# Kernel tuning notes

Hardware: AMD Instinct MI355X
Metric: run time of the kernel (lower is better)

The kernel has to match this reference:

```python
import jax, jax.numpy as jnp
import numpy as np

N = 4096   # nodes
E = 65536  # edges
D_IN = 64
H = 128
T = 8
B = 8


def setup_inputs() -> dict:
    key = jax.random.key(0)
    ks = jax.random.split(key, 6)
    x = jax.random.normal(ks[0], (B, T, N, D_IN), jnp.float32)
    edge_index = jax.random.randint(ks[1], (2, E), 0, N, dtype=jnp.int32)
    W0 = jax.random.normal(ks[2], (D_IN + H, 4 * H), jnp.float32) * 0.05
    b0 = jax.random.normal(ks[3], (4 * H,), jnp.float32) * 0.05
    W1 = jax.random.normal(ks[4], (H + H, 4 * H), jnp.float32) * 0.05
    b1 = jax.random.normal(ks[5], (4 * H,), jnp.float32) * 0.05
    return {"x": x, "W0": W0, "b0": b0, "W1": W1, "b1": b1, "edge_index": edge_index}


def _gcn_norm(edge_index, n):
    # PyG GCNConv(improved=True): A_hat = A + 2I, deg over incoming edges (col)
    src, dst = edge_index[0], edge_index[1]
    deg = jax.ops.segment_sum(jnp.ones(edge_index.shape[1], jnp.float32), dst, num_segments=n) + 2.0
    dinv = jax.lax.rsqrt(deg)  # deg >= 2 always, safe
    return src, dst, dinv


def _gcn_gates(comb, W, b, src, dst, dinv, n):
    # comb: (b, n, i+h) -> gates: (b, n, 4h)
    xw = jnp.einsum('bnf,fg->bng', comb, W)
    norm_e = dinv[src] * dinv[dst]                      # (E,)
    msgs = xw[:, src, :] * norm_e[None, :, None]        # (b, E, 4h)
    agg = jax.vmap(lambda m: jax.ops.segment_sum(m, dst, num_segments=n))(msgs)
    # self-loop with weight 2: norm = 2 * dinv[i]^2
    agg = agg + (2.0 * dinv * dinv)[None, :, None] * xw + b
    return agg


def reference(x, W0, b0, W1, b1, edge_index):
    src, dst, dinv = _gcn_norm(edge_index, N)

    def run_layer(seq, W, b):
        h_dim = W.shape[1] // 4

        def step(carry, xt):
            h, c = carry
            comb = jnp.concatenate([xt, h], axis=-1)
            gates = _gcn_gates(comb, W, b, src, dst, dinv, N)
            ci, cf, co, cg = jnp.split(gates, 4, axis=-1)
            i = jax.nn.sigmoid(ci)
            f = jax.nn.sigmoid(cf)
            o = jax.nn.sigmoid(co)
            g = jnp.tanh(cg)
            c_next = f * c + i * g
            h_next = o * jnp.tanh(c_next)
            return (h_next, c_next), h_next

        h0 = jnp.zeros((seq.shape[1], N, h_dim), seq.dtype)
        _, hs = jax.lax.scan(step, (h0, h0), seq)
        return hs  # (t, b, n, h)

    seq = jnp.swapaxes(x, 0, 1)  # batch_first -> (t, b, n, d)
    hs0 = run_layer(seq, W0, b0)
    hs1 = run_layer(hs0, W1, b1)
    return jnp.swapaxes(hs1, 0, 1)  # (b, t, n, h) last-layer output sequence
```

## Files before the change

kernel.cpp:

```cpp
#include <hip/hip_runtime.h>
#include <hip/hip_fp16.h>
#include <math.h>

constexpr int N_NODES = 4096;
constexpr int N_EDGES = 65536;
constexpr int D_INF   = 64;
constexpr int H       = 128;
constexpr int T       = 8;
constexpr int B       = 8;
constexpr int M       = B * N_NODES;

typedef __attribute__((ext_vector_type(8))) short bf16x8;
typedef __attribute__((ext_vector_type(4))) float f32x4;
typedef __attribute__((ext_vector_type(8))) _Float16 f16x8;
typedef __attribute__((ext_vector_type(4))) _Float16 f16x4;

__device__ inline unsigned short f2bf(float x) {
  unsigned int u = __float_as_uint(x);
  unsigned int r = (u + 0x7fffu + ((u >> 16) & 1u)) >> 16;
  return (unsigned short)r;
}
__device__ inline float bf2f(unsigned short b) {
  return __uint_as_float((unsigned int)b << 16);
}
__device__ __forceinline__ int swz(int s) { return s ^ (((s >> 7) & 7) << 3); }


__global__ void k_count(const int* __restrict__ dst, int* __restrict__ cnt) {
  int e = blockIdx.x * blockDim.x + threadIdx.x;
  if (e < N_EDGES) atomicAdd(&cnt[dst[e]], 1);
}

__global__ void k_dinv(const int* __restrict__ cnt, float* __restrict__ dinv) {
  int n = blockIdx.x * blockDim.x + threadIdx.x;
  if (n < N_NODES) dinv[n] = 1.0f / sqrtf((float)cnt[n] + 2.0f);
}

__global__ void k_scan(const int* __restrict__ cnt, int* __restrict__ rowptr) {
  __shared__ int sums[1024];
  int t = threadIdx.x;
  int v0 = cnt[4*t+0], v1 = cnt[4*t+1], v2 = cnt[4*t+2], v3 = cnt[4*t+3];
  int s0 = v0, s1 = s0 + v1, s2 = s1 + v2, s3 = s2 + v3;
  sums[t] = s3;
  __syncthreads();
  for (int off = 1; off < 1024; off <<= 1) {
    int x = (t >= off) ? sums[t - off] : 0;
    __syncthreads();
    sums[t] += x;
    __syncthreads();
  }
  int base = (t > 0) ? sums[t - 1] : 0;
  if (t == 0) rowptr[0] = 0;
  rowptr[4*t+1] = base + s0;
  rowptr[4*t+2] = base + s1;
  rowptr[4*t+3] = base + s2;
  rowptr[4*t+4] = base + s3;
}

__global__ void k_fill(const int* __restrict__ src, const int* __restrict__ dst,
                       const float* __restrict__ dinv, const int* __restrict__ rowptr,
                       int* __restrict__ fill, int2* __restrict__ eg) {
  int e = blockIdx.x * blockDim.x + threadIdx.x;
  if (e >= N_EDGES) return;
  int s = src[e], d = dst[e];
  int p = rowptr[d] + atomicAdd(&fill[d], 1);
  eg[p] = make_int2(s, __float_as_int(dinv[s] * dinv[d]));
}

__global__ void k_hist(const int* __restrict__ cnt, int* __restrict__ hist) {
  int n = blockIdx.x * blockDim.x + threadIdx.x;
  if (n < N_NODES) atomicAdd(&hist[min(cnt[n], 127)], 1);
}

__global__ void k_hscan(const int* __restrict__ hist, int* __restrict__ hbase) {
  __shared__ int sh[128];
  int t = threadIdx.x;
  sh[t] = hist[t];
  __syncthreads();
  for (int off = 1; off < 128; off <<= 1) {
    int x = (t >= off) ? sh[t - off] : 0;
    __syncthreads();
    sh[t] += x;
    __syncthreads();
  }
  hbase[t] = sh[t] - hist[t];
}

__global__ void k_place(const int* __restrict__ cnt, const int* __restrict__ hbase,
                        int* __restrict__ filld, int* __restrict__ sorted) {
  int n = blockIdx.x * blockDim.x + threadIdx.x;
  if (n >= N_NODES) return;
  int d = min(cnt[n], 127);
  sorted[hbase[d] + atomicAdd(&filld[d], 1)] = n;
}

__global__ void k_pack(const float* __restrict__ W, unsigned short* __restrict__ Bp,
                       int K) {
  int tid = blockIdx.x * 256 + threadIdx.x;
  if (tid >= K * 64) return;
  int lane = tid & 63;
  int ntg  = (tid >> 6) & 31;
  int kb   = tid >> 11;
  int gate = ntg & 3, fg = ntg >> 2;
  int corig = gate * 128 + fg * 16 + (lane & 15);
  int k0 = kb * 32 + (lane >> 4) * 8;
  long obase = ((long)(kb * 32 + ntg) * 64 + lane) * 8;
  long plane = (long)K * 512;
  #pragma unroll
  for (int j = 0; j < 8; ++j) {
    float v = W[(long)(k0 + j) * 512 + corig];
    unsigned short h = f2bf(v);
    Bp[obase + j]         = h;
    Bp[plane + obase + j] = f2bf(v - bf2f(h));
  }
}

__global__ __launch_bounds__(256) void k_ax(
    const int* __restrict__ rowptr, const int2* __restrict__ eg,
    const float* __restrict__ dinv, const float* __restrict__ x,
    _Float16* __restrict__ AX) {
  int tid = threadIdx.x;
  int grp = blockIdx.x * 16 + (tid >> 4);
  int l   = tid & 15;
  int c4  = l * 4;
  int n   = grp & (N_NODES - 1);
  int bt  = grp >> 12;
  int b   = bt & 7, tt = bt >> 3;
  const float* Xb = x + (long)(b * T + tt) * N_NODES * D_INF;
  float acc[4] = {0.f, 0.f, 0.f, 0.f};
  int rs = rowptr[n], re = rowptr[n + 1];
  int e = rs;
  for (; e + 3 < re; e += 4) {
    int2 q0 = eg[e], q1 = eg[e + 1], q2 = eg[e + 2], q3 = eg[e + 3];
    float w0 = __int_as_float(q0.y), w1 = __int_as_float(q1.y);
    float w2 = __int_as_float(q2.y), w3 = __int_as_float(q3.y);
    f32x4 a0 = *(const f32x4*)(Xb + (long)q0.x * D_INF + c4);
    f32x4 a1 = *(const f32x4*)(Xb + (long)q1.x * D_INF + c4);
    f32x4 a2 = *(const f32x4*)(Xb + (long)q2.x * D_INF + c4);
    f32x4 a3 = *(const f32x4*)(Xb + (long)q3.x * D_INF + c4);
    #pragma unroll
    for (int q = 0; q < 4; ++q)
      acc[q] += w0 * a0[q] + w1 * a1[q] + w2 * a2[q] + w3 * a3[q];
  }
  for (; e < re; ++e) {
    int2 q0 = eg[e];
    float w0 = __int_as_float(q0.y);
    f32x4 a0 = *(const f32x4*)(Xb + (long)q0.x * D_INF + c4);
    #pragma unroll
    for (int q = 0; q < 4; ++q) acc[q] += w0 * a0[q];
  }
  float dn = dinv[n];
  float sw = 2.0f * dn * dn;
  f32x4 a = *(const f32x4*)(Xb + (long)n * D_INF + c4);
  #pragma unroll
  for (int q = 0; q < 4; ++q) acc[q] += sw * a[q];
  f16x4 o;
  #pragma unroll
  for (int q = 0; q < 4; ++q) o[q] = (_Float16)acc[q];
  *(f16x4*)(AX + ((long)(tt * 8 + b) * N_NODES + n) * D_INF + c4) = o;
}

__global__ __launch_bounds__(512, 4) void k_l0(
    const int* __restrict__ sorted,
    const _Float16* __restrict__ AXt,
    const unsigned short* __restrict__ AH0,
    const unsigned short* __restrict__ Bp, const float* __restrict__ bias,
    _Float16* __restrict__ hout, float* __restrict__ cbuf) {
  __shared__ __align__(16) unsigned short Atx[8 * 2 * 64 * 8];
  __shared__ int nodeLDS[64];
  int tid  = threadIdx.x;
  int lane = tid & 63;
  int w    = tid >> 6;
  int j    = blockIdx.x;
  int b    = j & 7;
  int jj   = j >> 3;
  int g    = lane >> 4, l = lane & 15;
  int c4   = l * 4;
  int kbA32  = c4 >> 5;
  int subA32 = (l & 7) >> 1;
  int j0A32  = (l & 1) * 4;

  #pragma unroll
  for (int nd = 0; nd < 2; ++nd) {
    int r = (w << 3) + (g << 1) + nd;
    int pairIdx = jj * 32 + (r >> 1);
    int n = (r & 1) ? sorted[N_NODES - 1 - pairIdx] : sorted[pairIdx];
    if (l == 0) nodeLDS[r] = n;
    f16x4 xv = *(const f16x4*)(AXt + ((long)b * N_NODES + n) * D_INF + c4);
    unsigned long long hv = 0ull, lv = 0ull;
    #pragma unroll
    for (int q = 0; q < 4; ++q) {
      float a = (float)xv[q];
      unsigned short hs = f2bf(a);
      unsigned short ls = f2bf(a - bf2f(hs));
      hv |= (unsigned long long)hs << (16 * q);
      lv |= (unsigned long long)ls << (16 * q);
    }
    int mt = r >> 4;
    int lA = (r & 15) + 16 * subA32;
    *(unsigned long long*)(Atx + swz(((mt * 2 + kbA32) * 64 + lA) * 8 + j0A32)) = hv;
    *(unsigned long long*)(Atx + swz((((4 + mt) * 2 + kbA32) * 64 + lA) * 8 + j0A32)) = lv;
  }
  __syncthreads();

  int l15 = lane & 15, lq = lane >> 4;
  const unsigned short* bb  = Bp + (long)(w * 4) * 512 + lane * 8;
  const unsigned short* blp = bb + (long)192 * 512;

  f32x4 acc[4][4];
  #pragma unroll
  for (int mt = 0; mt < 4; ++mt)
    #pragma unroll
    for (int gt = 0; gt < 4; ++gt)
      acc[mt][gt] = (f32x4){0.f, 0.f, 0.f, 0.f};

  __builtin_amdgcn_s_setprio(1);
  #pragma unroll
  for (int kb = 0; kb < 6; ++kb) {
    bf16x8 AH_[4], AL_[4];
    if (kb < 2) {
      #pragma unroll
      for (int mt = 0; mt < 4; ++mt) {
        AH_[mt] = *(const bf16x8*)(Atx + swz(((mt * 2 + kb) * 64 + lane) * 8));
        AL_[mt] = *(const bf16x8*)(Atx + swz((((4 + mt) * 2 + kb) * 64 + lane) * 8));
      }
    } else {
      #pragma unroll
      for (int mt = 0; mt < 4; ++mt) {
        AH_[mt] = *(const bf16x8*)(AH0 + ((((long)j * 8 + mt) * 4 + (kb - 2)) * 64 + lane) * 8);
        AL_[mt] = *(const bf16x8*)(AH0 + ((((long)j * 8 + 4 + mt) * 4 + (kb - 2)) * 64 + lane) * 8);
      }
    }
    bf16x8 BH[4], BL[4];
    #pragma unroll
    for (int gt = 0; gt < 4; ++gt) {
      BH[gt] = *(const bf16x8*)(bb  + ((long)kb * 32 + gt) * 512);
      BL[gt] = *(const bf16x8*)(blp + ((long)kb * 32 + gt) * 512);
    }
    #pragma unroll
    for (int gt = 0; gt < 4; ++gt) {
      #pragma unroll
      for (int mt = 0; mt < 4; ++mt) {
        acc[mt][gt] = __builtin_amdgcn_mfma_f32_16x16x32_bf16(AH_[mt], BH[gt], acc[mt][gt], 0, 0, 0);
        acc[mt][gt] = __builtin_amdgcn_mfma_f32_16x16x32_bf16(AL_[mt], BH[gt], acc[mt][gt], 0, 0, 0);
        acc[mt][gt] = __builtin_amdgcn_mfma_f32_16x16x32_bf16(AH_[mt], BL[gt], acc[mt][gt], 0, 0, 0);
      }
    }
  }
  __builtin_amdgcn_s_setprio(0);

  int f = w * 16 + l15;
  float bi = bias[f], bff = bias[128 + f], bo = bias[256 + f], bg = bias[384 + f];
  #pragma unroll
  for (int mt = 0; mt < 4; ++mt) {
    #pragma unroll
    for (int r = 0; r < 4; ++r) {
      int rt = mt * 16 + lq * 4 + r;
      int n2 = nodeLDS[rt];
      float vi = 1.0f / (1.0f + __expf(-(acc[mt][0][r] + bi)));
      float vf = 1.0f / (1.0f + __expf(-(acc[mt][1][r] + bff)));
      float vo = 1.0f / (1.0f + __expf(-(acc[mt][2][r] + bo)));
      float vg = tanhf(acc[mt][3][r] + bg);
      long idx = ((long)b * N_NODES + n2) * H + f;
      float cn = vf * cbuf[idx] + vi * vg;
      float hn = vo * tanhf(cn);
      cbuf[idx] = cn;
      hout[idx] = (_Float16)hn;
    }
  }
}

__global__ __launch_bounds__(512, 4) void k_l1(
    const int* __restrict__ rowptr, const int2* __restrict__ eg,
    const float* __restrict__ dinv, const int* __restrict__ sorted,
    const _Float16* __restrict__ H0,
    const _Float16* __restrict__ H1r,
    const unsigned short* __restrict__ Bp, const float* __restrict__ bias,
    unsigned short* __restrict__ AH0,
    _Float16* __restrict__ h1out, float* __restrict__ cbuf,
    float* __restrict__ out2, int t) {
  constexpr int KB = 8;
  __shared__ __align__(16) unsigned short At[8 * KB * 64 * 8];
  __shared__ int nodeLDS[64];
  int tid  = threadIdx.x;
  int lane = tid & 63;
  int w    = tid >> 6;
  int j    = blockIdx.x;
  int b    = j & 7;
  int jj   = j >> 3;
  int g    = lane >> 4, l = lane & 15;
  int c8   = l * 8;
  const _Float16* A_p = H0  + (long)b * N_NODES * H;
  const _Float16* B_p = H1r + (long)b * N_NODES * H;
  int lane2f = 16 * (l & 3);
  int kbA16  = c8 >> 5;
  int kbB    = 4 + kbA16;

  #pragma unroll
  for (int nd = 0; nd < 2; ++nd) {
    int r  = (w << 3) + (g << 1) + nd;
    int pairIdx = jj * 32 + (r >> 1);
    int n  = (r & 1) ? sorted[N_NODES - 1 - pairIdx] : sorted[pairIdx];
    if (l == 0) nodeLDS[r] = n;
    int rs = rowptr[n], re = rowptr[n + 1];
    float accA[8] = {0.f,0.f,0.f,0.f,0.f,0.f,0.f,0.f};
    float accB[8] = {0.f,0.f,0.f,0.f,0.f,0.f,0.f,0.f};
    int e = rs;
    for (; e + 3 < re; e += 4) {
      int2 q0 = eg[e], q1 = eg[e + 1], q2 = eg[e + 2], q3 = eg[e + 3];
      float w0 = __int_as_float(q0.y), w1 = __int_as_float(q1.y);
      float w2 = __int_as_float(q2.y), w3 = __int_as_float(q3.y);
      f16x8 a0 = *(const f16x8*)(A_p + (long)q0.x * H + c8);
      f16x8 a1 = *(const f16x8*)(A_p + (long)q1.x * H + c8);
      f16x8 a2 = *(const f16x8*)(A_p + (long)q2.x * H + c8);
      f16x8 a3 = *(const f16x8*)(A_p + (long)q3.x * H + c8);
      #pragma unroll
      for (int q = 0; q < 8; ++q)
        accA[q] += w0 * (float)a0[q] + w1 * (float)a1[q]
                 + w2 * (float)a2[q] + w3 * (float)a3[q];
      f16x8 b0 = *(const f16x8*)(B_p + (long)q0.x * H + c8);
      f16x8 b1 = *(const f16x8*)(B_p + (long)q1.x * H + c8);
      f16x8 b2 = *(const f16x8*)(B_p + (long)q2.x * H + c8);
      f16x8 b3 = *(const f16x8*)(B_p + (long)q3.x * H + c8);
      #pragma unroll
      for (int q = 0; q < 8; ++q)
        accB[q] += w0 * (float)b0[q] + w1 * (float)b1[q]
                 + w2 * (float)b2[q] + w3 * (float)b3[q];
    }
    for (; e < re; ++e) {
      int2 q0 = eg[e];
      float w0 = __int_as_float(q0.y);
      f16x8 a0 = *(const f16x8*)(A_p + (long)q0.x * H + c8);
      #pragma unroll
      for (int q = 0; q < 8; ++q) accA[q] += w0 * (float)a0[q];
      f16x8 b0 = *(const f16x8*)(B_p + (long)q0.x * H + c8);
      #pragma unroll
      for (int q = 0; q < 8; ++q) accB[q] += w0 * (float)b0[q];
    }
    float dn = dinv[n];
    float sw = 2.0f * dn * dn;
    {
      f16x8 a = *(const f16x8*)(A_p + (long)n * H + c8);
      f16x8 v = *(const f16x8*)(B_p + (long)n * H + c8);
      #pragma unroll
      for (int q = 0; q < 8; ++q) {
        accA[q] += sw * (float)a[q];
        accB[q] += sw * (float)v[q];
      }
    }

    int mt    = r >> 4;
    int lane2 = (r & 15) + lane2f;
    {
      bf16x8 hv, lv;
      #pragma unroll
      for (int q = 0; q < 8; ++q) {
        unsigned short hs = f2bf(accB[q]);
        hv[q] = (short)hs;
        lv[q] = (short)f2bf(accB[q] - bf2f(hs));
      }
      *(bf16x8*)(At + swz((((mt)     * KB + kbB) * 64 + lane2) * 8)) = hv;
      *(bf16x8*)(At + swz((((4 + mt) * KB + kbB) * 64 + lane2) * 8)) = lv;
    }
    {
      bf16x8 hv, lv;
      #pragma unroll
      for (int q = 0; q < 8; ++q) {
        unsigned short hs = f2bf(accA[q]);
        hv[q] = (short)hs;
        lv[q] = (short)f2bf(accA[q] - bf2f(hs));
      }
      *(bf16x8*)(At + swz((((mt)     * KB + kbA16) * 64 + lane2) * 8)) = hv;
      *(bf16x8*)(At + swz((((4 + mt) * KB + kbA16) * 64 + lane2) * 8)) = lv;
      *(bf16x8*)(AH0 + ((((long)j * 8 + mt)     * 4 + kbA16) * 64 + lane2) * 8) = hv;
      *(bf16x8*)(AH0 + ((((long)j * 8 + 4 + mt) * 4 + kbA16) * 64 + lane2) * 8) = lv;
    }
  }
  __syncthreads();

  int l15 = lane & 15, lq = lane >> 4;
  const unsigned short* bb  = Bp + (long)(w * 4) * 512 + lane * 8;
  const unsigned short* blp = bb + (long)256 * 512;

  f32x4 acc[4][4];
  #pragma unroll
  for (int mt = 0; mt < 4; ++mt)
    #pragma unroll
    for (int gt = 0; gt < 4; ++gt)
      acc[mt][gt] = (f32x4){0.f, 0.f, 0.f, 0.f};

  __builtin_amdgcn_s_setprio(1);
  #pragma unroll 2
  for (int kb = 0; kb < KB; ++kb) {
    bf16x8 AH_[4], AL_[4];
    #pragma unroll
    for (int mt = 0; mt < 4; ++mt) {
      AH_[mt] = *(const bf16x8*)(At + swz((((mt)     * KB + kb) * 64 + lane) * 8));
      AL_[mt] = *(const bf16x8*)(At + swz((((4 + mt) * KB + kb) * 64 + lane) * 8));
    }
    bf16x8 BH[4], BL[4];
    #pragma unroll
    for (int gt = 0; gt < 4; ++gt) {
      BH[gt] = *(const bf16x8*)(bb  + ((long)kb * 32 + gt) * 512);
      BL[gt] = *(const bf16x8*)(blp + ((long)kb * 32 + gt) * 512);
    }
    #pragma unroll
    for (int gt = 0; gt < 4; ++gt) {
      #pragma unroll
      for (int mt = 0; mt < 4; ++mt) {
        acc[mt][gt] = __builtin_amdgcn_mfma_f32_16x16x32_bf16(AH_[mt], BH[gt], acc[mt][gt], 0, 0, 0);
        acc[mt][gt] = __builtin_amdgcn_mfma_f32_16x16x32_bf16(AL_[mt], BH[gt], acc[mt][gt], 0, 0, 0);
        acc[mt][gt] = __builtin_amdgcn_mfma_f32_16x16x32_bf16(AH_[mt], BL[gt], acc[mt][gt], 0, 0, 0);
      }
    }
  }
  __builtin_amdgcn_s_setprio(0);

  int f = w * 16 + l15;
  float bi = bias[f], bff = bias[128 + f], bo = bias[256 + f], bg = bias[384 + f];
  #pragma unroll
  for (int mt = 0; mt < 4; ++mt) {
    #pragma unroll
    for (int r = 0; r < 4; ++r) {
      int rt = mt * 16 + lq * 4 + r;
      int n2 = nodeLDS[rt];
      float vi = 1.0f / (1.0f + __expf(-(acc[mt][0][r] + bi)));
      float vf = 1.0f / (1.0f + __expf(-(acc[mt][1][r] + bff)));
      float vo = 1.0f / (1.0f + __expf(-(acc[mt][2][r] + bo)));
      float vg = tanhf(acc[mt][3][r] + bg);
      long idx = ((long)b * N_NODES + n2) * H + f;
      float cn = vf * cbuf[idx] + vi * vg;
      float hn = vo * tanhf(cn);
      cbuf[idx] = cn;
      h1out[idx] = (_Float16)hn;
      __builtin_nontemporal_store(hn,
          &out2[(((long)b * T + t) * N_NODES + n2) * H + f]);
    }
  }
}


extern "C" void kernel_launch(void* const* d_in, const int* in_sizes, int n_in,
                              void* d_out, int out_size, void* d_ws, size_t ws_size,
                              hipStream_t stream) {
  const float* x  = (const float*)d_in[0];
  const float* W0 = (const float*)d_in[1];
  const float* b0 = (const float*)d_in[2];
  const float* W1 = (const float*)d_in[3];
  const float* b1 = (const float*)d_in[4];
  const int*   ei = (const int*)d_in[5];
  const int* srcp = ei;
  const int* dstp = ei + N_EDGES;
  float* out = (float*)d_out;

  char* p = (char*)d_ws;
  auto alloc = [&](size_t bytes) {
    char* r = p;
    p += (bytes + 255) & ~(size_t)255;
    return r;
  };
  int*   cnt    = (int*)  alloc(N_NODES * 4);
  int*   fill   = (int*)  alloc(N_NODES * 4);
  float* dinv   = (float*)alloc(N_NODES * 4);
  int*   rowptr = (int*)  alloc((N_NODES + 1) * 4);
  int2*  eg     = (int2*) alloc((size_t)N_EDGES * 8);
  int*   hist   = (int*)  alloc(128 * 4);
  int*   hbase  = (int*)  alloc(128 * 4);
  int*   filld  = (int*)  alloc(128 * 4);
  int*   sorted = (int*)  alloc(N_NODES * 4);
  float* cc     = (float*)alloc((size_t)2 * M * H * 4);
  _Float16* hh  = (_Float16*)alloc((size_t)3 * M * H * 2);
  _Float16* AX  = (_Float16*)alloc((size_t)T * M * D_INF * 2);
  unsigned short* AH0 = (unsigned short*)alloc((size_t)512 * 8 * 4 * 64 * 8 * 2);
  unsigned short* Bp0 = (unsigned short*)alloc((size_t)192 * 512 * 2 * 2);
  unsigned short* Bp1 = (unsigned short*)alloc((size_t)256 * 512 * 2 * 2);
  float*    c0  = cc;
  float*    c1  = cc + (size_t)M * H;
  _Float16* h0  = hh;
  _Float16* h1a = hh + (size_t)M * H;
  _Float16* h1b = hh + (size_t)2 * M * H;

  hipMemsetAsync(cnt,   0, N_NODES * 4, stream);
  hipMemsetAsync(fill,  0, N_NODES * 4, stream);
  hipMemsetAsync(hist,  0, 128 * 4, stream);
  hipMemsetAsync(filld, 0, 128 * 4, stream);
  hipMemsetAsync(cc,    0, (size_t)2 * M * H * 4, stream);
  hipMemsetAsync(hh,    0, (size_t)3 * M * H * 2, stream);
  hipMemsetAsync(AH0,   0, (size_t)512 * 8 * 4 * 64 * 8 * 2, stream);

  k_count<<<N_EDGES / 256, 256, 0, stream>>>(dstp, cnt);
  k_dinv <<<N_NODES / 256, 256, 0, stream>>>(cnt, dinv);
  k_scan <<<1, 1024, 0, stream>>>(cnt, rowptr);
  k_fill <<<N_EDGES / 256, 256, 0, stream>>>(srcp, dstp, dinv, rowptr, fill, eg);
  k_hist <<<N_NODES / 256, 256, 0, stream>>>(cnt, hist);
  k_hscan<<<1, 128, 0, stream>>>(hist, hbase);
  k_place<<<N_NODES / 256, 256, 0, stream>>>(cnt, hbase, filld, sorted);
  k_pack <<<(192 * 64 + 255) / 256, 256, 0, stream>>>(W0, Bp0, 192);
  k_pack <<<(256 * 64 + 255) / 256, 256, 0, stream>>>(W1, Bp1, 256);
  k_ax   <<<(8 * T * N_NODES) / 16, 256, 0, stream>>>(rowptr, eg, dinv, x, AX);

  for (int t = 0; t < T; ++t) {
    const _Float16* h1r = (t & 1) ? h1b : h1a;
    _Float16*       h1w = (t & 1) ? h1a : h1b;
    k_l0<<<512, 512, 0, stream>>>(sorted,
        AX + (size_t)t * M * D_INF, AH0, Bp0, b0, h0, c0);
    k_l1<<<512, 512, 0, stream>>>(rowptr, eg, dinv, sorted,
        h0, h1r, Bp1, b1, AH0, h1w, c1, out, t);
  }
}
```

Baseline: 829.5 us.

## Precompute A·X in MFMA-fragment bf16 hi/lo layout, batch all timesteps per edge

The A·X aggregation kernel now handles all 8 timesteps per node and batch, so each edge's index and weight are read once and reused across timesteps. It writes the result directly as split bf16 hi/lo fragments in the swizzle-free MFMA operand layout, indexed by each node's rank in the degree-sorted order, using a new rank kernel. The layer-0 step kernel therefore drops its LDS staging and per-step fp16-to-bf16 split conversion and loads A fragments straight from global memory. In exchange the AX buffer doubles in size, and k_ax keeps 32 accumulators per thread, which raises register pressure.

```diff
diff --git a/kernel.cpp b/kernel.cpp
--- a/kernel.cpp
+++ b/kernel.cpp
@@ -9,11 +9,11 @@
 constexpr int T       = 8;
 constexpr int B       = 8;
 constexpr int M       = B * N_NODES;
+constexpr long AXF_T  = 512L * 8 * 2 * 64 * 8;
 
 typedef __attribute__((ext_vector_type(8))) short bf16x8;
 typedef __attribute__((ext_vector_type(4))) float f32x4;
 typedef __attribute__((ext_vector_type(8))) _Float16 f16x8;
-typedef __attribute__((ext_vector_type(4))) _Float16 f16x4;
 
 __device__ inline unsigned short f2bf(float x) {
   unsigned int u = __float_as_uint(x);
@@ -94,6 +94,11 @@
   sorted[hbase[d] + atomicAdd(&filld[d], 1)] = n;
 }
 
+__global__ void k_rank(const int* __restrict__ sorted, int* __restrict__ rank) {
+  int p = blockIdx.x * 256 + threadIdx.x;
+  if (p < N_NODES) rank[sorted[p]] = p;
+}
+
 __global__ void k_pack(const float* __restrict__ W, unsigned short* __restrict__ Bp,
                        int K) {
   int tid = blockIdx.x * 256 + threadIdx.x;
@@ -115,58 +120,94 @@
   }
 }
 
-__global__ __launch_bounds__(256) void k_ax(
+__global__ void k_ax(
     const int* __restrict__ rowptr, const int2* __restrict__ eg,
-    const float* __restrict__ dinv, const float* __restrict__ x,
-    _Float16* __restrict__ AX) {
+    const float* __restrict__ dinv, const int* __restrict__ rank,
+    const float* __restrict__ x, unsigned short* __restrict__ AXf) {
   int tid = threadIdx.x;
-  int grp = blockIdx.x * 16 + (tid >> 4);
   int l   = tid & 15;
+  int b   = blockIdx.x & 7;
+  int n   = (blockIdx.x >> 3) * 16 + (tid >> 4);
   int c4  = l * 4;
-  int n   = grp & (N_NODES - 1);
-  int bt  = grp >> 12;
-  int b   = bt & 7, tt = bt >> 3;
-  const float* Xb = x + (long)(b * T + tt) * N_NODES * D_INF;
-  float acc[4] = {0.f, 0.f, 0.f, 0.f};
+  constexpr long TS = (long)N_NODES * D_INF;
+  const float* xb = x + (long)b * T * TS + c4;
+  float acc[8][4];
+  #pragma unroll
+  for (int tt = 0; tt < 8; ++tt)
+    #pragma unroll
+    for (int q = 0; q < 4; ++q) acc[tt][q] = 0.f;
+
   int rs = rowptr[n], re = rowptr[n + 1];
   int e = rs;
-  for (; e + 3 < re; e += 4) {
-    int2 q0 = eg[e], q1 = eg[e + 1], q2 = eg[e + 2], q3 = eg[e + 3];
+  for (; e + 1 < re; e += 2) {
+    int2 q0 = eg[e], q1 = eg[e + 1];
     float w0 = __int_as_float(q0.y), w1 = __int_as_float(q1.y);
-    float w2 = __int_as_float(q2.y), w3 = __int_as_float(q3.y);
-    f32x4 a0 = *(const f32x4*)(Xb + (long)q0.x * D_INF + c4);
-    f32x4 a1 = *(const f32x4*)(Xb + (long)q1.x * D_INF + c4);
-    f32x4 a2 = *(const f32x4*)(Xb + (long)q2.x * D_INF + c4);
-    f32x4 a3 = *(const f32x4*)(Xb + (long)q3.x * D_INF + c4);
-    #pragma unroll
-    for (int q = 0; q < 4; ++q)
-      acc[q] += w0 * a0[q] + w1 * a1[q] + w2 * a2[q] + w3 * a3[q];
-  }
-  for (; e < re; ++e) {
+    const float* p0 = xb + (long)q0.x * D_INF;
+    const float* p1 = xb + (long)q1.x * D_INF;
+    #pragma unroll
+    for (int tt = 0; tt < 8; ++tt) {
+      f32x4 v0 = *(const f32x4*)(p0 + tt * TS);
+      f32x4 v1 = *(const f32x4*)(p1 + tt * TS);
+      #pragma unroll
+      for (int q = 0; q < 4; ++q) acc[tt][q] += w0 * v0[q] + w1 * v1[q];
+    }
+  }
+  if (e < re) {
     int2 q0 = eg[e];
     float w0 = __int_as_float(q0.y);
-    f32x4 a0 = *(const f32x4*)(Xb + (long)q0.x * D_INF + c4);
-    #pragma unroll
-    for (int q = 0; q < 4; ++q) acc[q] += w0 * a0[q];
+    const float* p0 = xb + (long)q0.x * D_INF;
+    #pragma unroll
+    for (int tt = 0; tt < 8; ++tt) {
+      f32x4 v0 = *(const f32x4*)(p0 + tt * TS);
+      #pragma unroll
+      for (int q = 0; q < 4; ++q) acc[tt][q] += w0 * v0[q];
+    }
   }
   float dn = dinv[n];
   float sw = 2.0f * dn * dn;
-  f32x4 a = *(const f32x4*)(Xb + (long)n * D_INF + c4);
-  #pragma unroll
-  for (int q = 0; q < 4; ++q) acc[q] += sw * a[q];
-  f16x4 o;
-  #pragma unroll
-  for (int q = 0; q < 4; ++q) o[q] = (_Float16)acc[q];
-  *(f16x4*)(AX + ((long)(tt * 8 + b) * N_NODES + n) * D_INF + c4) = o;
+  {
+    const float* ps = xb + (long)n * D_INF;
+    #pragma unroll
+    for (int tt = 0; tt < 8; ++tt) {
+      f32x4 v = *(const f32x4*)(ps + tt * TS);
+      #pragma unroll
+      for (int q = 0; q < 4; ++q) acc[tt][q] += sw * v[q];
+    }
+  }
+
+  int p  = rank[n];
+  int side = (p >= N_NODES / 2) ? 1 : 0;
+  int pairIdx = side ? (N_NODES - 1 - p) : p;
+  int jj = pairIdx >> 5;
+  int r  = ((pairIdx & 31) << 1) | side;
+  int j  = jj * 8 + b;
+  int mt = r >> 4;
+  int lA = (r & 15) + 16 * ((l & 7) >> 1);
+  int j0 = (l & 1) * 4;
+  int kb = l >> 3;
+  long base_hi = ((((long)j * 8 + mt)     * 2 + kb) * 64 + lA) * 8 + j0;
+  long base_lo = ((((long)j * 8 + 4 + mt) * 2 + kb) * 64 + lA) * 8 + j0;
+  #pragma unroll
+  for (int tt = 0; tt < 8; ++tt) {
+    unsigned long long hv = 0ull, lv = 0ull;
+    #pragma unroll
+    for (int q = 0; q < 4; ++q) {
+      unsigned short hs = f2bf(acc[tt][q]);
+      unsigned short ls = f2bf(acc[tt][q] - bf2f(hs));
+      hv |= (unsigned long long)hs << (16 * q);
+      lv |= (unsigned long long)ls << (16 * q);
+    }
+    *(unsigned long long*)(AXf + tt * AXF_T + base_hi) = hv;
+    *(unsigned long long*)(AXf + tt * AXF_T + base_lo) = lv;
+  }
 }
 
 __global__ __launch_bounds__(512, 4) void k_l0(
     const int* __restrict__ sorted,
-    const _Float16* __restrict__ AXt,
+    const unsigned short* __restrict__ AXf_t,
     const unsigned short* __restrict__ AH0,
     const unsigned short* __restrict__ Bp, const float* __restrict__ bias,
     _Float16* __restrict__ hout, float* __restrict__ cbuf) {
-  __shared__ __align__(16) unsigned short Atx[8 * 2 * 64 * 8];
   __shared__ int nodeLDS[64];
   int tid  = threadIdx.x;
   int lane = tid & 63;
@@ -174,32 +215,9 @@
   int j    = blockIdx.x;
   int b    = j & 7;
   int jj   = j >> 3;
-  int g    = lane >> 4, l = lane & 15;
-  int c4   = l * 4;
-  int kbA32  = c4 >> 5;
-  int subA32 = (l & 7) >> 1;
-  int j0A32  = (l & 1) * 4;
-
-  #pragma unroll
-  for (int nd = 0; nd < 2; ++nd) {
-    int r = (w << 3) + (g << 1) + nd;
-    int pairIdx = jj * 32 + (r >> 1);
-    int n = (r & 1) ? sorted[N_NODES - 1 - pairIdx] : sorted[pairIdx];
-    if (l == 0) nodeLDS[r] = n;
-    f16x4 xv = *(const f16x4*)(AXt + ((long)b * N_NODES + n) * D_INF + c4);
-    unsigned long long hv = 0ull, lv = 0ull;
-    #pragma unroll
-    for (int q = 0; q < 4; ++q) {
-      float a = (float)xv[q];
-      unsigned short hs = f2bf(a);
-      unsigned short ls = f2bf(a - bf2f(hs));
-      hv |= (unsigned long long)hs << (16 * q);
-      lv |= (unsigned long long)ls << (16 * q);
-    }
-    int mt = r >> 4;
-    int lA = (r & 15) + 16 * subA32;
-    *(unsigned long long*)(Atx + swz(((mt * 2 + kbA32) * 64 + lA) * 8 + j0A32)) = hv;
-    *(unsigned long long*)(Atx + swz((((4 + mt) * 2 + kbA32) * 64 + lA) * 8 + j0A32)) = lv;
+  if (tid < 64) {
+    int pairIdx = jj * 32 + (tid >> 1);
+    nodeLDS[tid] = (tid & 1) ? sorted[N_NODES - 1 - pairIdx] : sorted[pairIdx];
   }
   __syncthreads();
 
@@ -221,13 +239,13 @@
     if (kb < 2) {
       #pragma unroll
       for (int mt = 0; mt < 4; ++mt) {
-        AH_[mt] = *(const bf16x8*)(Atx + swz(((mt * 2 + kb) * 64 + lane) * 8));
-        AL_[mt] = *(const bf16x8*)(Atx + swz((((4 + mt) * 2 + kb) * 64 + lane) * 8));
+        AH_[mt] = *(const bf16x8*)(AXf_t + ((((long)j * 8 + mt)     * 2 + kb) * 64 + lane) * 8);
+        AL_[mt] = *(const bf16x8*)(AXf_t + ((((long)j * 8 + 4 + mt) * 2 + kb) * 64 + lane) * 8);
       }
     } else {
       #pragma unroll
       for (int mt = 0; mt < 4; ++mt) {
-        AH_[mt] = *(const bf16x8*)(AH0 + ((((long)j * 8 + mt) * 4 + (kb - 2)) * 64 + lane) * 8);
+        AH_[mt] = *(const bf16x8*)(AH0 + ((((long)j * 8 + mt)     * 4 + (kb - 2)) * 64 + lane) * 8);
         AL_[mt] = *(const bf16x8*)(AH0 + ((((long)j * 8 + 4 + mt) * 4 + (kb - 2)) * 64 + lane) * 8);
       }
     }
@@ -468,9 +486,10 @@
   int*   hbase  = (int*)  alloc(128 * 4);
   int*   filld  = (int*)  alloc(128 * 4);
   int*   sorted = (int*)  alloc(N_NODES * 4);
+  int*   rankb  = (int*)  alloc(N_NODES * 4);
   float* cc     = (float*)alloc((size_t)2 * M * H * 4);
   _Float16* hh  = (_Float16*)alloc((size_t)3 * M * H * 2);
-  _Float16* AX  = (_Float16*)alloc((size_t)T * M * D_INF * 2);
+  unsigned short* AXf = (unsigned short*)alloc((size_t)T * AXF_T * 2);
   unsigned short* AH0 = (unsigned short*)alloc((size_t)512 * 8 * 4 * 64 * 8 * 2);
   unsigned short* Bp0 = (unsigned short*)alloc((size_t)192 * 512 * 2 * 2);
   unsigned short* Bp1 = (unsigned short*)alloc((size_t)256 * 512 * 2 * 2);
@@ -495,15 +514,16 @@
   k_hist <<<N_NODES / 256, 256, 0, stream>>>(cnt, hist);
   k_hscan<<<1, 128, 0, stream>>>(hist, hbase);
   k_place<<<N_NODES / 256, 256, 0, stream>>>(cnt, hbase, filld, sorted);
+  k_rank <<<N_NODES / 256, 256, 0, stream>>>(sorted, rankb);
   k_pack <<<(192 * 64 + 255) / 256, 256, 0, stream>>>(W0, Bp0, 192);
   k_pack <<<(256 * 64 + 255) / 256, 256, 0, stream>>>(W1, Bp1, 256);
-  k_ax   <<<(8 * T * N_NODES) / 16, 256, 0, stream>>>(rowptr, eg, dinv, x, AX);
+  k_ax   <<<2048, 256, 0, stream>>>(rowptr, eg, dinv, rankb, x, AXf);
 
   for (int t = 0; t < T; ++t) {
     const _Float16* h1r = (t & 1) ? h1b : h1a;
     _Float16*       h1w = (t & 1) ? h1a : h1b;
     k_l0<<<512, 512, 0, stream>>>(sorted,
-        AX + (size_t)t * M * D_INF, AH0, Bp0, b0, h0, c0);
+        AXf + (size_t)t * AXF_T, AH0, Bp0, b0, h0, c0);
     k_l1<<<512, 512, 0, stream>>>(rowptr, eg, dinv, sorted,
         h0, h1r, Bp1, b1, AH0, h1w, c1, out, t);
   }
```

Result: slower. 848.5 us (+2.3%).
